# Performance work log

Measured on AMD Instinct MI355X. Metric: run time of the kernel, lower is better.

The kernel has to match this reference:

```python
import jax, jax.numpy as jnp
import numpy as np

B, T, D, H = 4, 2048, 1024, 16
HD = D // H


def setup_inputs() -> dict:
    key = jax.random.key(0)
    ks = jax.random.split(key, 6)
    x = jax.random.normal(ks[0], (B, T, D), dtype=jnp.float32)
    entity_bias = jax.random.normal(ks[1], (B, T, T), dtype=jnp.float32) * 0.02
    W_qkv = jax.random.normal(ks[2], (D, 3 * D), dtype=jnp.float32) * (1.0 / np.sqrt(D))
    b_qkv = jnp.zeros((3 * D,), dtype=jnp.float32)
    W_out = jax.random.normal(ks[3], (D, D), dtype=jnp.float32) * (1.0 / np.sqrt(D))
    b_out = jnp.zeros((D,), dtype=jnp.float32)
    return {"x": x, "entity_bias": entity_bias, "W_qkv": W_qkv, "b_qkv": b_qkv,
            "W_out": W_out, "b_out": b_out}


def reference(x, entity_bias, W_qkv, b_qkv, W_out, b_out):
    b, t, d = x.shape
    hd = d // H
    scale = hd ** -0.5
    qkv = x @ W_qkv + b_qkv                      # [B,T,3D]
    q, k, v = jnp.split(qkv, 3, axis=-1)
    sh = lambda z: z.reshape(b, t, H, hd).transpose(0, 2, 1, 3)  # [B,H,T,hd]
    q, k, v = sh(q), sh(k), sh(v)
    w = jnp.einsum('bhqd,bhkd->bhqk', q, k) * scale
    w = w + entity_bias[:, None]                 # broadcast over heads
    causal = jnp.triu(jnp.ones((t, t), dtype=bool), k=1)
    w = jnp.where(causal[None, None], jnp.float32(-1e9), w)
    a = jax.nn.softmax(w, axis=-1)
    out = jnp.einsum('bhqk,bhkd->bhqd', a, v)    # [B,H,T,hd]
    out = out.transpose(0, 2, 1, 3).reshape(b, t, d)
    return out @ W_out + b_out
```

## Files before the change

### kernel.cpp

```cpp
#include <hip/hip_runtime.h>

typedef __attribute__((ext_vector_type(8))) short short8;
typedef __attribute__((ext_vector_type(4))) short short4v;
typedef __attribute__((ext_vector_type(4))) float f32x4;

#define B_  4
#define T_  2048
#define D_  1024
#define H_  16
#define HD_ 64

#define LOG2E 1.4426950408889634f
#define QSCALE 0.1803368801111243f

__device__ __forceinline__ short f2bf(float f) {
  unsigned u = __builtin_bit_cast(unsigned, f);
  u = (u + 0x7FFFu + ((u >> 16) & 1u)) >> 16;
  return (short)u;
}
__device__ __forceinline__ short f2bf_trunc(float f) {
  return (short)(__builtin_bit_cast(unsigned, f) >> 16);
}
__device__ __forceinline__ float bf2f(short s) {
  unsigned u = ((unsigned)(unsigned short)s) << 16;
  return __builtin_bit_cast(float, u);
}

__device__ __forceinline__ void g2l16(const void* g, void* l) {
  __builtin_amdgcn_global_load_lds((const __attribute__((address_space(1))) void*)g,
                                   (__attribute__((address_space(3))) void*)l, 16, 0, 0);
}

__global__ __launch_bounds__(256) void cast_x_kernel(const float* __restrict__ src,
                                                     short* __restrict__ dst) {
  int i = (blockIdx.x * 256 + threadIdx.x) * 4;
  float4 v = *(const float4*)(src + i);
  short4v o;
  o.x = f2bf(v.x); o.y = f2bf(v.y); o.z = f2bf(v.z); o.w = f2bf(v.w);
  *(short4v*)(dst + i) = o;
}

__global__ __launch_bounds__(256) void tcast_kernel(const float* __restrict__ src,
                                                    short* __restrict__ dst, int R, int C) {
  __shared__ float tile[32][33];
  int cb = blockIdx.x, rb = blockIdx.y;
  int tr = threadIdx.x >> 5, tc = threadIdx.x & 31;
#pragma unroll
  for (int p = 0; p < 4; ++p) {
    int r = p * 8 + tr;
    tile[r][tc] = src[(size_t)(rb * 32 + r) * C + cb * 32 + tc];
  }
  __syncthreads();
#pragma unroll
  for (int p = 0; p < 4; ++p) {
    int r = p * 8 + tr;
    dst[(size_t)(cb * 32 + r) * R + rb * 32 + tc] = f2bf(tile[tc][r]);
  }
}

__global__ __launch_bounds__(512) void pb_kernel(const float* __restrict__ bias,
                                                 short* __restrict__ PB) {
  int bid = blockIdx.x;
  int b = bid / 136, tidx = bid % 136;
  int qt = 0, base = 0;
  while (base + qt + 1 <= tidx) { base += qt + 1; ++qt; }
  int kt = tidx - base;
  int tid = threadIdx.x;
  int w = tid >> 6, lane = tid & 63, quad = lane >> 4, l15 = lane & 15;
  short vals[32];
#pragma unroll
  for (int tj = 0; tj < 8; ++tj)
#pragma unroll
    for (int rr = 0; rr < 4; ++rr) {
      int ql = w * 16 + quad * 4 + rr;
      int kl = tj * 16 + l15;
      float v = bias[((size_t)b * T_ + qt * 128 + ql) * T_ + kt * 128 + kl] * LOG2E;
      if (kt == qt && kl > ql) v = -1.0e9f;
      vals[tj * 4 + rr] = f2bf(v);
    }
  short* dst = PB + ((size_t)bid * 512 + tid) * 32;
#pragma unroll
  for (int j = 0; j < 4; ++j) *(short8*)(dst + j * 8) = *(const short8*)(vals + j * 8);
}

__device__ __forceinline__ void gemm_stage(const short* __restrict__ A,
                                           const short* __restrict__ Bt, int K, int mb, int nb,
                                           int kk, short* As, short* Bs, int wave, int lane) {
#pragma unroll
  for (int i = 0; i < 2; ++i) {
    int sbase = i * 256 + wave * 64;
    int s = sbase + lane;
    int kc = s >> 7, r = s & 127;
    g2l16(A + (size_t)(mb * 128 + r) * K + kk * 32 + kc * 8, As + sbase * 8);
    g2l16(Bt + (size_t)(nb * 128 + r) * K + kk * 32 + kc * 8, Bs + sbase * 8);
  }
}

__device__ __forceinline__ void gemm_compute(const short* As, const short* Bs, f32x4 acc[4][4],
                                             int quad, int l15, int wr, int wc) {
  short8 af[4], bq[4];
#pragma unroll
  for (int t = 0; t < 4; ++t) {
    af[t] = *(const short8*)(As + (quad * 128 + wr * 64 + t * 16 + l15) * 8);
    bq[t] = *(const short8*)(Bs + (quad * 128 + wc * 64 + t * 16 + l15) * 8);
  }
#pragma unroll
  for (int i = 0; i < 4; ++i)
#pragma unroll
    for (int j = 0; j < 4; ++j)
      acc[i][j] = __builtin_amdgcn_mfma_f32_16x16x32_bf16(af[i], bq[j], acc[i][j], 0, 0, 0);
}

__device__ __forceinline__ void gemm_core(const short* __restrict__ A, const short* __restrict__ Bt,
                                          int K, int mb, int nb, short* As, short* Bs,
                                          f32x4 acc[4][4]) {
  const int tid = threadIdx.x;
  const int wave = tid >> 6, lane = tid & 63;
  const int quad = lane >> 4, l15 = lane & 15;
  const int wr = wave >> 1, wc = wave & 1;
  f32x4 zero = {0.f, 0.f, 0.f, 0.f};
#pragma unroll
  for (int i = 0; i < 4; ++i)
#pragma unroll
    for (int j = 0; j < 4; ++j) acc[i][j] = zero;

  const int nK = K >> 5;
  gemm_stage(A, Bt, K, mb, nb, 0, As, Bs, wave, lane);
  __syncthreads();
  for (int kk = 0; kk < nK - 1; ++kk) {
    int cur = kk & 1;
    gemm_stage(A, Bt, K, mb, nb, kk + 1, As + (cur ^ 1) * 4096, Bs + (cur ^ 1) * 4096, wave, lane);
    gemm_compute(As + cur * 4096, Bs + cur * 4096, acc, quad, l15, wr, wc);
    __syncthreads();
  }
  gemm_compute(As + ((nK - 1) & 1) * 4096, Bs + ((nK - 1) & 1) * 4096, acc, quad, l15, wr, wc);
}

__global__ __launch_bounds__(256, 3) void gemm_qkv_kernel(
    const short* __restrict__ xb, const short* __restrict__ Wqt, const float* __restrict__ bqkv,
    short* __restrict__ Qb, short* __restrict__ Kb, short* __restrict__ Vt) {
  __shared__ alignas(16) short As[2 * 4096];
  __shared__ alignas(16) short Bs[2 * 4096];
  f32x4 acc[4][4];
  int nb = blockIdx.x, mb = blockIdx.y;
  gemm_core(xb, Wqt, D_, mb, nb, As, Bs, acc);

  const int tid = threadIdx.x, wave = tid >> 6, lane = tid & 63;
  const int quad = lane >> 4, l15 = lane & 15;
  const int wr = wave >> 1, wc = wave & 1;
  int part = nb >> 3;
  int h = ((nb & 7) << 1) + wc;
  if (part == 2) {
#pragma unroll
    for (int j = 0; j < 4; ++j) {
      int n = nb * 128 + wc * 64 + j * 16 + l15;
      int hd = j * 16 + l15;
      float bv = bqkv[n];
#pragma unroll
      for (int i = 0; i < 4; ++i) {
        int m0 = mb * 128 + wr * 64 + i * 16 + quad * 4;
        int b = m0 >> 11, t0 = m0 & 2047;
        short4v pv;
#pragma unroll
        for (int rr = 0; rr < 4; ++rr) pv[rr] = f2bf(acc[i][j][rr] + bv);
        *(short4v*)(Vt + ((size_t)((b * H_ + h) * HD_ + hd)) * T_ + t0) = pv;
      }
    }
  } else {
    short* dst = (part == 0) ? Qb : Kb;
    float sc = (part == 0) ? QSCALE : 1.0f;
#pragma unroll
    for (int j = 0; j < 4; ++j) {
      int n = nb * 128 + wc * 64 + j * 16 + l15;
      int hd = j * 16 + l15;
      float bv = bqkv[n];
#pragma unroll
      for (int i = 0; i < 4; ++i) {
        int mrow = mb * 128 + wr * 64 + i * 16 + quad * 4;
#pragma unroll
        for (int rr = 0; rr < 4; ++rr) {
          int m = mrow + rr;
          int b = m >> 11, t = m & 2047;
          dst[((size_t)((b * H_ + h) * T_ + t)) * HD_ + hd] = f2bf((acc[i][j][rr] + bv) * sc);
        }
      }
    }
  }
}

__global__ __launch_bounds__(256, 3) void gemm_out_kernel(
    const short* __restrict__ Ob, const short* __restrict__ Wot,
    const float* __restrict__ bout, float* __restrict__ out) {
  __shared__ alignas(16) short As[2 * 4096];
  __shared__ alignas(16) short Bs[2 * 4096];
  f32x4 acc[4][4];
  int nb = blockIdx.x, mb = blockIdx.y;
  gemm_core(Ob, Wot, D_, mb, nb, As, Bs, acc);

  const int tid = threadIdx.x, wave = tid >> 6, lane = tid & 63;
  const int quad = lane >> 4, l15 = lane & 15;
  const int wr = wave >> 1, wc = wave & 1;
#pragma unroll
  for (int j = 0; j < 4; ++j) {
    int n = nb * 128 + wc * 64 + j * 16 + l15;
    float bv = bout[n];
#pragma unroll
    for (int i = 0; i < 4; ++i) {
      int mrow = mb * 128 + wr * 64 + i * 16 + quad * 4;
#pragma unroll
      for (int rr = 0; rr < 4; ++rr) {
        out[(size_t)(mrow + rr) * D_ + n] = acc[i][j][rr] + bv;
      }
    }
  }
}

__global__ __launch_bounds__(512, 2) void attn_kernel(
    const short* __restrict__ Qb, const short* __restrict__ Kb, const short* __restrict__ Vt,
    const short* __restrict__ PB, short* __restrict__ Ob) {
  __shared__ alignas(16) short Ks[2][8192];
  __shared__ alignas(16) short Vs[2][8192];
  __shared__ alignas(16) short Ps[8][512];

  const int tid = threadIdx.x, wave = tid >> 6, lane = tid & 63;
  const int quad = lane >> 4, l15 = lane & 15;
  const int bh = blockIdx.x;
  const int pair = blockIdx.y;
  const int qa = pair, qb = 15 - pair;
  const int b = bh >> 4, h = bh & 15;

  short8 aqA[2], aqB[2];
#pragma unroll
  for (int i = 0; i < 2; ++i) {
    int sbase = i * 512 + wave * 64;
    int s = sbase + lane;
    g2l16(Qb + ((size_t)bh * T_ + qa * 128 + (s & 127)) * HD_ + (s >> 7) * 8, &Ks[0][0] + sbase * 8);
    g2l16(Qb + ((size_t)bh * T_ + qb * 128 + (s & 127)) * HD_ + (s >> 7) * 8, &Vs[0][0] + sbase * 8);
  }
  __syncthreads();
#pragma unroll
  for (int c2 = 0; c2 < 2; ++c2) {
    aqA[c2] = *(const short8*)(&Ks[0][0] + ((c2 * 4 + quad) * 128 + wave * 16 + l15) * 8);
    aqB[c2] = *(const short8*)(&Vs[0][0] + ((c2 * 4 + quad) * 128 + wave * 16 + l15) * 8);
  }
  __syncthreads();

  f32x4 zero = {0.f, 0.f, 0.f, 0.f};
  f32x4 oA[4], oB[4];
  float liA[4], liB[4];
#pragma unroll
  for (int hj = 0; hj < 4; ++hj) { oA[hj] = zero; oB[hj] = zero; }
#pragma unroll
  for (int rr = 0; rr < 4; ++rr) { liA[rr] = 0.f; liB[rr] = 0.f; }

  const short* pbA = PB + ((size_t)(b * 136 + ((qa * (qa + 1)) >> 1)) * 512 + tid) * 32;
  const short* pbB = PB + ((size_t)(b * 136 + ((qb * (qb + 1)) >> 1)) * 512 + tid) * 32;
  short* pw = &Ps[wave][0];

  auto stage_kv = [&](int kt, int bufc) {
#pragma unroll
    for (int i = 0; i < 2; ++i) {
      int sbase = i * 512 + wave * 64;
      int s = sbase + lane;
      g2l16(Kb + ((size_t)bh * T_ + kt * 128 + (s & 127)) * HD_ + (s >> 7) * 8,
            &Ks[bufc][0] + sbase * 8);
      g2l16(Vt + ((size_t)bh * HD_ + (s & 63)) * T_ + kt * 128 + (s >> 6) * 8,
            &Vs[bufc][0] + sbase * 8);
    }
  };

  auto attn_step = [&](int kt, int bufc) {
    const short* Ksc = &Ks[bufc][0];
    const short* Vsc = &Vs[bufc][0];
#pragma unroll
    for (int tile = 0; tile < 2; ++tile) {
      if (tile == 1 && kt > qa) break;
      const short* pp = (tile == 0 ? pbB : pbA) + (size_t)kt * (512 * 32);
      const short8* aq = (tile == 0) ? aqB : aqA;
      f32x4* o = (tile == 0) ? oB : oA;
      float* li = (tile == 0) ? liB : liA;

      f32x4 sc[8];
#pragma unroll
      for (int j4 = 0; j4 < 4; ++j4) {
        short8 pb = *(const short8*)(pp + j4 * 8);
#pragma unroll
        for (int tp = 0; tp < 2; ++tp)
#pragma unroll
          for (int rr = 0; rr < 4; ++rr) sc[j4 * 2 + tp][rr] = bf2f(pb[tp * 4 + rr]);
      }
#pragma unroll
      for (int tj = 0; tj < 8; ++tj) {
        short8 bk0 = *(const short8*)(Ksc + (quad * 128 + tj * 16 + l15) * 8);
        short8 bk1 = *(const short8*)(Ksc + ((4 + quad) * 128 + tj * 16 + l15) * 8);
        sc[tj] = __builtin_amdgcn_mfma_f32_16x16x32_bf16(aq[0], bk0, sc[tj], 0, 0, 0);
        sc[tj] = __builtin_amdgcn_mfma_f32_16x16x32_bf16(aq[1], bk1, sc[tj], 0, 0, 0);
      }

#pragma unroll
      for (int tj = 0; tj < 8; ++tj)
#pragma unroll
        for (int rr = 0; rr < 4; ++rr) {
          float p = __builtin_amdgcn_exp2f(sc[tj][rr]);
          sc[tj][rr] = p;
          li[rr] += p;
        }

#pragma unroll
      for (int kc = 0; kc < 4; ++kc) {
#pragma unroll
        for (int tp = 0; tp < 2; ++tp) {
          int tj = kc * 2 + tp;
          int klc = tp * 16 + l15;
          int hi = (klc >> 3) * 16;
#pragma unroll
          for (int rr = 0; rr < 4; ++rr) {
            pw[(hi + quad * 4 + rr) * 8 + (klc & 7)] = f2bf_trunc(sc[tj][rr]);
          }
        }
        short8 ap = *(const short8*)(pw + (quad * 16 + l15) * 8);
#pragma unroll
        for (int hj = 0; hj < 4; ++hj) {
          short8 bv = *(const short8*)(Vsc + ((kc * 4 + quad) * 64 + hj * 16 + l15) * 8);
          o[hj] = __builtin_amdgcn_mfma_f32_16x16x32_bf16(ap, bv, o[hj], 0, 0, 0);
        }
      }
    }
  };

  stage_kv(0, 0);
  __syncthreads();
  for (int kt = 0; kt < qb; ++kt) {
    int cur = kt & 1;
    stage_kv(kt + 1, cur ^ 1);
    attn_step(kt, cur);
    __syncthreads();
  }
  attn_step(qb, qb & 1);

#pragma unroll
  for (int d = 1; d < 16; d <<= 1)
#pragma unroll
    for (int rr = 0; rr < 4; ++rr) {
      liA[rr] += __shfl_xor(liA[rr], d, 64);
      liB[rr] += __shfl_xor(liB[rr], d, 64);
    }

#pragma unroll
  for (int hj = 0; hj < 4; ++hj)
#pragma unroll
    for (int rr = 0; rr < 4; ++rr) {
      int qrow = wave * 16 + quad * 4 + rr;
      int dcol = h * 64 + hj * 16 + l15;
      Ob[((size_t)b * T_ + qa * 128 + qrow) * D_ + dcol] = f2bf(oA[hj][rr] / liA[rr]);
      Ob[((size_t)b * T_ + qb * 128 + qrow) * D_ + dcol] = f2bf(oB[hj][rr] / liB[rr]);
    }
}

extern "C" void kernel_launch(void* const* d_in, const int* in_sizes, int n_in,
                              void* d_out, int out_size, void* d_ws, size_t ws_size,
                              hipStream_t stream) {
  const float* x    = (const float*)d_in[0];
  const float* bias = (const float*)d_in[1];
  const float* Wqkv = (const float*)d_in[2];
  const float* bqkv = (const float*)d_in[3];
  const float* Wout = (const float*)d_in[4];
  const float* bout = (const float*)d_in[5];
  float* out = (float*)d_out;
  char* ws = (char*)d_ws;

  short* xb   = (short*)(ws + 0);
  short* Ob   = (short*)(ws + 0);
  short* Wqt  = (short*)(ws + 16777216);
  short* Wot  = (short*)(ws + 23068672);
  short* Qb   = (short*)(ws + 25165824);
  short* Kb   = (short*)(ws + 41943040);
  short* Vt   = (short*)(ws + 58720256);
  short* PB   = (short*)(ws + 75497472);

  cast_x_kernel<<<8192, 256, 0, stream>>>(x, xb);
  tcast_kernel<<<dim3(96, 32), 256, 0, stream>>>(Wqkv, Wqt, 1024, 3072);
  tcast_kernel<<<dim3(32, 32), 256, 0, stream>>>(Wout, Wot, 1024, 1024);
  pb_kernel<<<544, 512, 0, stream>>>(bias, PB);
  gemm_qkv_kernel<<<dim3(24, 64), 256, 0, stream>>>(xb, Wqt, bqkv, Qb, Kb, Vt);
  attn_kernel<<<dim3(64, 8), 512, 0, stream>>>(Qb, Kb, Vt, PB, Ob);
  gemm_out_kernel<<<dim3(8, 64), 256, 0, stream>>>(Ob, Wot, bout, out);
}
```

Before: 406.0 us.

## Swizzle LDS layouts for GEMM and attention, hoist bias loads, raise occupancy

```diff
diff --git a/kernel.cpp b/kernel.cpp
--- a/kernel.cpp
+++ b/kernel.cpp
@@ -90,19 +90,21 @@
   for (int i = 0; i < 2; ++i) {
     int sbase = i * 256 + wave * 64;
     int s = sbase + lane;
-    int kc = s >> 7, r = s & 127;
-    g2l16(A + (size_t)(mb * 128 + r) * K + kk * 32 + kc * 8, As + sbase * 8);
-    g2l16(Bt + (size_t)(nb * 128 + r) * K + kk * 32 + kc * 8, Bs + sbase * 8);
+    int r = s >> 2;
+    int cg = (s & 3) ^ ((s >> 3) & 3);
+    g2l16(A + (size_t)(mb * 128 + r) * K + kk * 32 + cg * 8, As + sbase * 8);
+    g2l16(Bt + (size_t)(nb * 128 + r) * K + kk * 32 + cg * 8, Bs + sbase * 8);
   }
 }
 
 __device__ __forceinline__ void gemm_compute(const short* As, const short* Bs, f32x4 acc[4][4],
                                              int quad, int l15, int wr, int wc) {
   short8 af[4], bq[4];
+  int sw = quad ^ ((l15 >> 1) & 3);
 #pragma unroll
   for (int t = 0; t < 4; ++t) {
-    af[t] = *(const short8*)(As + (quad * 128 + wr * 64 + t * 16 + l15) * 8);
-    bq[t] = *(const short8*)(Bs + (quad * 128 + wc * 64 + t * 16 + l15) * 8);
+    af[t] = *(const short8*)(As + ((wr * 64 + t * 16 + l15) * 4 + sw) * 8);
+    bq[t] = *(const short8*)(Bs + ((wc * 64 + t * 16 + l15) * 4 + sw) * 8);
   }
 #pragma unroll
   for (int i = 0; i < 4; ++i)
@@ -136,7 +138,7 @@
   gemm_compute(As + ((nK - 1) & 1) * 4096, Bs + ((nK - 1) & 1) * 4096, acc, quad, l15, wr, wc);
 }
 
-__global__ __launch_bounds__(256, 3) void gemm_qkv_kernel(
+__global__ __launch_bounds__(256, 4) void gemm_qkv_kernel(
     const short* __restrict__ xb, const short* __restrict__ Wqt, const float* __restrict__ bqkv,
     short* __restrict__ Qb, short* __restrict__ Kb, short* __restrict__ Vt) {
   __shared__ alignas(16) short As[2 * 4096];
@@ -188,7 +190,7 @@
   }
 }
 
-__global__ __launch_bounds__(256, 3) void gemm_out_kernel(
+__global__ __launch_bounds__(256, 4) void gemm_out_kernel(
     const short* __restrict__ Ob, const short* __restrict__ Wot,
     const float* __restrict__ bout, float* __restrict__ out) {
   __shared__ alignas(16) short As[2 * 4096];
@@ -234,14 +236,20 @@
   for (int i = 0; i < 2; ++i) {
     int sbase = i * 512 + wave * 64;
     int s = sbase + lane;
-    g2l16(Qb + ((size_t)bh * T_ + qa * 128 + (s & 127)) * HD_ + (s >> 7) * 8, &Ks[0][0] + sbase * 8);
-    g2l16(Qb + ((size_t)bh * T_ + qb * 128 + (s & 127)) * HD_ + (s >> 7) * 8, &Vs[0][0] + sbase * 8);
+    int r = s >> 3;
+    int cg = (s & 7) ^ (r & 7);
+    g2l16(Qb + ((size_t)bh * T_ + qa * 128 + r) * HD_ + cg * 8, &Ks[0][0] + sbase * 8);
+    g2l16(Qb + ((size_t)bh * T_ + qb * 128 + r) * HD_ + cg * 8, &Vs[0][0] + sbase * 8);
   }
   __syncthreads();
-#pragma unroll
-  for (int c2 = 0; c2 < 2; ++c2) {
-    aqA[c2] = *(const short8*)(&Ks[0][0] + ((c2 * 4 + quad) * 128 + wave * 16 + l15) * 8);
-    aqB[c2] = *(const short8*)(&Vs[0][0] + ((c2 * 4 + quad) * 128 + wave * 16 + l15) * 8);
+  {
+    int qrow = wave * 16 + l15;
+#pragma unroll
+    for (int c2 = 0; c2 < 2; ++c2) {
+      int ch = (c2 * 4 + quad) ^ (l15 & 7);
+      aqA[c2] = *(const short8*)(&Ks[0][0] + (qrow * 8 + ch) * 8);
+      aqB[c2] = *(const short8*)(&Vs[0][0] + (qrow * 8 + ch) * 8);
+    }
   }
   __syncthreads();
 
@@ -262,37 +270,34 @@
     for (int i = 0; i < 2; ++i) {
       int sbase = i * 512 + wave * 64;
       int s = sbase + lane;
-      g2l16(Kb + ((size_t)bh * T_ + kt * 128 + (s & 127)) * HD_ + (s >> 7) * 8,
-            &Ks[bufc][0] + sbase * 8);
-      g2l16(Vt + ((size_t)bh * HD_ + (s & 63)) * T_ + kt * 128 + (s >> 6) * 8,
-            &Vs[bufc][0] + sbase * 8);
+      int rk = s >> 3, ck = (s & 7) ^ ((s >> 3) & 7);
+      g2l16(Kb + ((size_t)bh * T_ + kt * 128 + rk) * HD_ + ck * 8, &Ks[bufc][0] + sbase * 8);
+      int rv = s >> 4, cv = (s & 15) ^ ((s >> 4) & 7);
+      g2l16(Vt + ((size_t)bh * HD_ + rv) * T_ + kt * 128 + cv * 8, &Vs[bufc][0] + sbase * 8);
     }
   };
 
-  auto attn_step = [&](int kt, int bufc) {
+  auto attn_step = [&](int kt, int bufc, const short8* pBv, const short8* pAv) {
     const short* Ksc = &Ks[bufc][0];
     const short* Vsc = &Vs[bufc][0];
+    const int ks0 = quad ^ (l15 & 7), ks1 = ks0 ^ 4;
+    const int vsw = l15 & 7;
 #pragma unroll
     for (int tile = 0; tile < 2; ++tile) {
       if (tile == 1 && kt > qa) break;
-      const short* pp = (tile == 0 ? pbB : pbA) + (size_t)kt * (512 * 32);
+      const short8* pbv = (tile == 0) ? pBv : pAv;
       const short8* aq = (tile == 0) ? aqB : aqA;
       f32x4* o = (tile == 0) ? oB : oA;
       float* li = (tile == 0) ? liB : liA;
 
       f32x4 sc[8];
 #pragma unroll
-      for (int j4 = 0; j4 < 4; ++j4) {
-        short8 pb = *(const short8*)(pp + j4 * 8);
-#pragma unroll
-        for (int tp = 0; tp < 2; ++tp)
-#pragma unroll
-          for (int rr = 0; rr < 4; ++rr) sc[j4 * 2 + tp][rr] = bf2f(pb[tp * 4 + rr]);
-      }
+      for (int tj = 0; tj < 8; ++tj) sc[tj] = zero;
 #pragma unroll
       for (int tj = 0; tj < 8; ++tj) {
-        short8 bk0 = *(const short8*)(Ksc + (quad * 128 + tj * 16 + l15) * 8);
-        short8 bk1 = *(const short8*)(Ksc + ((4 + quad) * 128 + tj * 16 + l15) * 8);
+        int key = tj * 16 + l15;
+        short8 bk0 = *(const short8*)(Ksc + (key * 8 + ks0) * 8);
+        short8 bk1 = *(const short8*)(Ksc + (key * 8 + ks1) * 8);
         sc[tj] = __builtin_amdgcn_mfma_f32_16x16x32_bf16(aq[0], bk0, sc[tj], 0, 0, 0);
         sc[tj] = __builtin_amdgcn_mfma_f32_16x16x32_bf16(aq[1], bk1, sc[tj], 0, 0, 0);
       }
@@ -301,7 +306,7 @@
       for (int tj = 0; tj < 8; ++tj)
 #pragma unroll
         for (int rr = 0; rr < 4; ++rr) {
-          float p = __builtin_amdgcn_exp2f(sc[tj][rr]);
+          float p = __builtin_amdgcn_exp2f(sc[tj][rr] + bf2f(pbv[tj >> 1][(tj & 1) * 4 + rr]));
           sc[tj][rr] = p;
           li[rr] += p;
         }
@@ -321,7 +326,9 @@
         short8 ap = *(const short8*)(pw + (quad * 16 + l15) * 8);
 #pragma unroll
         for (int hj = 0; hj < 4; ++hj) {
-          short8 bv = *(const short8*)(Vsc + ((kc * 4 + quad) * 64 + hj * 16 + l15) * 8);
+          int hd = hj * 16 + l15;
+          int tc = (kc * 4 + quad) ^ vsw;
+          short8 bv = *(const short8*)(Vsc + (hd * 16 + tc) * 8);
           o[hj] = __builtin_amdgcn_mfma_f32_16x16x32_bf16(ap, bv, o[hj], 0, 0, 0);
         }
       }
@@ -333,10 +340,27 @@
   for (int kt = 0; kt < qb; ++kt) {
     int cur = kt & 1;
     stage_kv(kt + 1, cur ^ 1);
-    attn_step(kt, cur);
+    short8 pBv[4], pAv[4];
+    {
+      const short* ppB = pbB + (size_t)kt * (512 * 32);
+#pragma unroll
+      for (int j4 = 0; j4 < 4; ++j4) pBv[j4] = *(const short8*)(ppB + j4 * 8);
+      if (kt <= qa) {
+        const short* ppA = pbA + (size_t)kt * (512 * 32);
+#pragma unroll
+        for (int j4 = 0; j4 < 4; ++j4) pAv[j4] = *(const short8*)(ppA + j4 * 8);
+      }
+    }
+    attn_step(kt, cur, pBv, pAv);
     __syncthreads();
   }
-  attn_step(qb, qb & 1);
+  {
+    short8 pBv[4], pAv[4];
+    const short* ppB = pbB + (size_t)qb * (512 * 32);
+#pragma unroll
+    for (int j4 = 0; j4 < 4; ++j4) pBv[j4] = *(const short8*)(ppB + j4 * 8);
+    attn_step(qb, qb & 1, pBv, pAv);
+  }
 
 #pragma unroll
   for (int d = 1; d < 16; d <<= 1)
```

After: 462.2 us. 1.14x slower.
